# Kernel optimization log

Measured on AMD Instinct MI355X. Metric: run time of the kernel, lower is better.

## Reference

```python
import jax, jax.numpy as jnp
import numpy as np

N = 65536    # collocation points
N1 = 1024    # RBF centers
EPS = 0.1    # multiscale parameter used for width init scale


def setup_inputs() -> dict:
    key = jax.random.key(0)
    ks = jax.random.split(key, 10)
    x = jax.random.uniform(ks[0], (N, 2), dtype=jnp.float32)

    def mk(i):
        h = jax.random.uniform(ks[3 * i + 1], (N1,), dtype=jnp.float32)
        c = jax.random.uniform(ks[3 * i + 2], (N1, 2), dtype=jnp.float32)
        w = 5.0 * jax.random.uniform(ks[3 * i + 3], (N1, 2), dtype=jnp.float32) / EPS
        return h, c, w

    h1, c1, w1 = mk(0)
    h2, c2, w2 = mk(1)
    h3, c3, w3 = mk(2)
    return dict(x=x, hight=h1, center=c1, width=w1,
                hight2=h2, center2=c2, width2=w2,
                hight3=h3, center3=c3, width3=w3)


def _rbf(X, c, h, w):
    """Gaussian RBF expansion. X:(N,2) points, c:(N1,2) centers,
    h:(N1,) heights, w:(N1,2) widths. Returns u, du/dx, du/dy, each (N,)."""
    x1 = X[:, 0:1] - c[None, :, 0]          # (N, N1)
    y1 = X[:, 1:2] - c[None, :, 1]          # (N, N1)
    d1 = w[:, 0] ** 2                        # (N1,)
    d2 = w[:, 1] ** 2                        # (N1,)
    e = jnp.exp(-(x1 ** 2) * d1 - (y1 ** 2) * d2)  # (N, N1)
    u = e @ h                                # (N,)
    ux = (-2.0 * x1 * d1 * e) @ h            # (N,)
    uy = (-2.0 * y1 * d2 * e) @ h            # (N,)
    return u, ux, uy


def reference(x, hight, center, width, hight2, center2, width2,
              hight3, center3, width3):
    _, ux, uy = _rbf(x, center, hight, width)
    P, Px, _ = _rbf(x, center2, hight2, width2)
    Q, _, Qy = _rbf(x, center3, hight3, width3)
    return (ux, uy, P, Px, Q, Qy)
```

## Files before the change

### kernel.cpp

```cpp
#include <hip/hip_runtime.h>
#include <math.h>

#define N_PTS  65536
#define N_CTR  1024
#define CHUNK  128
#define PPT    4
#define PPB    (256 * PPT)

#if __has_builtin(__builtin_amdgcn_exp2f)
#define EXP2(v) __builtin_amdgcn_exp2f(v)
#else
#define EXP2(v) exp2f(v)
#endif


__global__ __launch_bounds__(256) void prep_kernel(
    const float* __restrict__ h0, const float* __restrict__ c0, const float* __restrict__ w0,
    const float* __restrict__ h1, const float* __restrict__ c1, const float* __restrict__ w1,
    const float* __restrict__ h2, const float* __restrict__ c2, const float* __restrict__ w2,
    float4* __restrict__ RA, float4* __restrict__ RB, float* __restrict__ RC,
    float4* __restrict__ out_zero)
{
    const int idx = blockIdx.x * 256 + threadIdx.x;

    {
        float4 z = make_float4(0.f, 0.f, 0.f, 0.f);
        float4* o = out_zero + idx * 32;
        #pragma unroll
        for (int t = 0; t < 32; ++t) o[t] = z;
    }

    if (idx >= 3 * N_CTR) return;
    const int set = idx >> 10;
    const int j   = idx & (N_CTR - 1);

    const float*  h = (set == 0) ? h0 : ((set == 1) ? h1 : h2);
    const float2* c = (const float2*)((set == 0) ? c0 : ((set == 1) ? c1 : c2));
    const float2* w = (const float2*)((set == 0) ? w0 : ((set == 1) ? w1 : w2));

    const float LOG2E = 1.4426950408889634f;
    float2 cj = c[j];
    float2 wj = w[j];
    float  hh = h[j];
    float d1 = wj.x * wj.x;
    float d2 = wj.y * wj.y;
    float zb =  2.f * cj.x * d1 * LOG2E;
    float zc = -d1 * LOG2E;
    float zd =  2.f * cj.y * d2 * LOG2E;
    float ze = -d2 * LOG2E;
    float za = -(cj.x * cj.x * d1 + cj.y * cj.y * d2) * LOG2E;
    float k0, k1, k2, k3;
    if (set == 0) {
        k0 = -2.f * hh * d1;  k1 = 2.f * hh * d1 * cj.x;
        k2 = -2.f * hh * d2;  k3 = 2.f * hh * d2 * cj.y;
    } else if (set == 1) {
        k0 = hh;  k1 = -2.f * hh * d1;  k2 = 2.f * hh * d1 * cj.x;  k3 = 0.f;
    } else {
        k0 = hh;  k1 = -2.f * hh * d2;  k2 = 2.f * hh * d2 * cj.y;  k3 = 0.f;
    }
    RA[idx] = make_float4(zb, zc, zd, ze);
    RB[idx] = make_float4(za, k0, k1, k2);
    RC[idx] = k3;
}

__global__ __launch_bounds__(256, 6) void srbf_main(
    const float* __restrict__ x,
    const float4* __restrict__ RA,
    const float4* __restrict__ RB,
    const float*  __restrict__ RC,
    float* __restrict__ out)
{
    const int bid   = blockIdx.x;
    const int set   = bid >> 9;
    const int r     = bid & 511;
    const int chunk = r >> 6;
    const int pblk  = r & 63;
    const int tid   = threadIdx.x;
    const int cbase = set * N_CTR + chunk * CHUNK;

    const int base = pblk * PPB + tid;
    float X[PPT], Y[PPT];
    #pragma unroll
    for (int p = 0; p < PPT; ++p) {
        float2 q = ((const float2*)x)[base + p * 256];
        X[p] = q.x;  Y[p] = q.y;
    }

    if (set == 0) {
        float A0[PPT], A1[PPT], A2[PPT], A3[PPT];
        #pragma unroll
        for (int p = 0; p < PPT; ++p) { A0[p] = A1[p] = A2[p] = A3[p] = 0.f; }

        #pragma unroll 4
        for (int jj = 0; jj < CHUNK; ++jj) {
            const float4 A  = RA[cbase + jj];
            const float4 B  = RB[cbase + jj];
            const float  k3 = RC[cbase + jj];
            float e[PPT];
            #pragma unroll
            for (int p = 0; p < PPT; ++p) {
                float t1 = fmaf(X[p], A.y, A.x);
                float t2 = fmaf(X[p], t1,  B.x);
                float t3 = fmaf(Y[p], A.w, A.z);
                float s  = fmaf(Y[p], t3,  t2);
                e[p] = EXP2(s);
            }
            #pragma unroll
            for (int p = 0; p < PPT; ++p) {
                A0[p] = fmaf(B.y, e[p], A0[p]);
                A1[p] = fmaf(B.z, e[p], A1[p]);
                A2[p] = fmaf(B.w, e[p], A2[p]);
                A3[p] = fmaf(k3,  e[p], A3[p]);
            }
        }
        #pragma unroll
        for (int p = 0; p < PPT; ++p) {
            const int i = base + p * 256;
            atomicAdd(&out[i],         fmaf(X[p], A0[p], A1[p]));
            atomicAdd(&out[N_PTS + i], fmaf(Y[p], A2[p], A3[p]));
        }
    } else {
        float A0[PPT], A1[PPT], A2[PPT];
        #pragma unroll
        for (int p = 0; p < PPT; ++p) { A0[p] = A1[p] = A2[p] = 0.f; }

        #pragma unroll 4
        for (int jj = 0; jj < CHUNK; ++jj) {
            const float4 A = RA[cbase + jj];
            const float4 B = RB[cbase + jj];
            float e[PPT];
            #pragma unroll
            for (int p = 0; p < PPT; ++p) {
                float t1 = fmaf(X[p], A.y, A.x);
                float t2 = fmaf(X[p], t1,  B.x);
                float t3 = fmaf(Y[p], A.w, A.z);
                float s  = fmaf(Y[p], t3,  t2);
                e[p] = EXP2(s);
            }
            #pragma unroll
            for (int p = 0; p < PPT; ++p) {
                A0[p] = fmaf(B.y, e[p], A0[p]);
                A1[p] = fmaf(B.z, e[p], A1[p]);
                A2[p] = fmaf(B.w, e[p], A2[p]);
            }
        }
        float* o = out + (size_t)set * 2 * N_PTS;
        #pragma unroll
        for (int p = 0; p < PPT; ++p) {
            const int i = base + p * 256;
            const float g = (set == 1) ? X[p] : Y[p];
            atomicAdd(&o[i],         A0[p]);
            atomicAdd(&o[N_PTS + i], fmaf(g, A1[p], A2[p]));
        }
    }
}

extern "C" void kernel_launch(void* const* d_in, const int* in_sizes, int n_in,
                              void* d_out, int out_size, void* d_ws, size_t ws_size,
                              hipStream_t stream) {
    const float* x  = (const float*)d_in[0];
    const float* h1 = (const float*)d_in[1];
    const float* c1 = (const float*)d_in[2];
    const float* w1 = (const float*)d_in[3];
    const float* h2 = (const float*)d_in[4];
    const float* c2 = (const float*)d_in[5];
    const float* w2 = (const float*)d_in[6];
    const float* h3 = (const float*)d_in[7];
    const float* c3 = (const float*)d_in[8];
    const float* w3 = (const float*)d_in[9];

    char* ws = (char*)d_ws;
    float4* RA = (float4*)(ws);
    float4* RB = (float4*)(ws + 49152);
    float*  RC = (float*) (ws + 98304);

    prep_kernel<<<dim3(12), dim3(256), 0, stream>>>(
        h1, c1, w1, h2, c2, w2, h3, c3, w3, RA, RB, RC, (float4*)d_out);

    srbf_main<<<dim3(1536), dim3(256), 0, stream>>>(x, RA, RB, RC, (float*)d_out);
}
```

Measured before the change: 60.73 us.

## Fuse center precompute into main kernel via shared memory, memset output

```diff
diff --git a/kernel.cpp b/kernel.cpp
--- a/kernel.cpp
+++ b/kernel.cpp
@@ -6,6 +6,7 @@
 #define CHUNK  128
 #define PPT    4
 #define PPB    (256 * PPT)
+#define LOG2E  1.4426950408889634f
 
 #if __has_builtin(__builtin_amdgcn_exp2f)
 #define EXP2(v) __builtin_amdgcn_exp2f(v)
@@ -13,70 +14,52 @@
 #define EXP2(v) exp2f(v)
 #endif
 
-
-__global__ __launch_bounds__(256) void prep_kernel(
+__global__ __launch_bounds__(256) void srbf_main(
+    const float* __restrict__ x,
     const float* __restrict__ h0, const float* __restrict__ c0, const float* __restrict__ w0,
     const float* __restrict__ h1, const float* __restrict__ c1, const float* __restrict__ w1,
     const float* __restrict__ h2, const float* __restrict__ c2, const float* __restrict__ w2,
-    float4* __restrict__ RA, float4* __restrict__ RB, float* __restrict__ RC,
-    float4* __restrict__ out_zero)
-{
-    const int idx = blockIdx.x * 256 + threadIdx.x;
-
-    {
-        float4 z = make_float4(0.f, 0.f, 0.f, 0.f);
-        float4* o = out_zero + idx * 32;
-        #pragma unroll
-        for (int t = 0; t < 32; ++t) o[t] = z;
-    }
-
-    if (idx >= 3 * N_CTR) return;
-    const int set = idx >> 10;
-    const int j   = idx & (N_CTR - 1);
-
-    const float*  h = (set == 0) ? h0 : ((set == 1) ? h1 : h2);
-    const float2* c = (const float2*)((set == 0) ? c0 : ((set == 1) ? c1 : c2));
-    const float2* w = (const float2*)((set == 0) ? w0 : ((set == 1) ? w1 : w2));
-
-    const float LOG2E = 1.4426950408889634f;
-    float2 cj = c[j];
-    float2 wj = w[j];
-    float  hh = h[j];
-    float d1 = wj.x * wj.x;
-    float d2 = wj.y * wj.y;
-    float zb =  2.f * cj.x * d1 * LOG2E;
-    float zc = -d1 * LOG2E;
-    float zd =  2.f * cj.y * d2 * LOG2E;
-    float ze = -d2 * LOG2E;
-    float za = -(cj.x * cj.x * d1 + cj.y * cj.y * d2) * LOG2E;
-    float k0, k1, k2, k3;
-    if (set == 0) {
-        k0 = -2.f * hh * d1;  k1 = 2.f * hh * d1 * cj.x;
-        k2 = -2.f * hh * d2;  k3 = 2.f * hh * d2 * cj.y;
-    } else if (set == 1) {
-        k0 = hh;  k1 = -2.f * hh * d1;  k2 = 2.f * hh * d1 * cj.x;  k3 = 0.f;
-    } else {
-        k0 = hh;  k1 = -2.f * hh * d2;  k2 = 2.f * hh * d2 * cj.y;  k3 = 0.f;
-    }
-    RA[idx] = make_float4(zb, zc, zd, ze);
-    RB[idx] = make_float4(za, k0, k1, k2);
-    RC[idx] = k3;
-}
-
-__global__ __launch_bounds__(256, 6) void srbf_main(
-    const float* __restrict__ x,
-    const float4* __restrict__ RA,
-    const float4* __restrict__ RB,
-    const float*  __restrict__ RC,
     float* __restrict__ out)
 {
+    __shared__ float4 sA[CHUNK];
+    __shared__ float4 sK[CHUNK];
+    __shared__ float  sk3[CHUNK];
+
     const int bid   = blockIdx.x;
     const int set   = bid >> 9;
     const int r     = bid & 511;
     const int chunk = r >> 6;
     const int pblk  = r & 63;
     const int tid   = threadIdx.x;
-    const int cbase = set * N_CTR + chunk * CHUNK;
+
+    if (tid < CHUNK) {
+        const int j = chunk * CHUNK + tid;
+        const float*  h = (set == 0) ? h0 : ((set == 1) ? h1 : h2);
+        const float2* c = (const float2*)((set == 0) ? c0 : ((set == 1) ? c1 : c2));
+        const float2* w = (const float2*)((set == 0) ? w0 : ((set == 1) ? w1 : w2));
+        float2 cj = c[j];
+        float2 wj = w[j];
+        float  hh = h[j];
+        float d1 = wj.x * wj.x;
+        float d2 = wj.y * wj.y;
+        float zb =  2.f * cj.x * d1 * LOG2E;
+        float zc = -d1 * LOG2E;
+        float zd =  2.f * cj.y * d2 * LOG2E;
+        float ze = -d2 * LOG2E;
+        float za = -(cj.x * cj.x * d1 + cj.y * cj.y * d2) * LOG2E;
+        float k0, k1, k2, k3;
+        if (set == 0) {
+            k0 = -2.f * hh * d1;  k1 = 2.f * hh * d1 * cj.x;
+            k2 = -2.f * hh * d2;  k3 = 2.f * hh * d2 * cj.y;
+        } else if (set == 1) {
+            k0 = hh;  k1 = -2.f * hh * d1;  k2 = 2.f * hh * d1 * cj.x;  k3 = 0.f;
+        } else {
+            k0 = hh;  k1 = -2.f * hh * d2;  k2 = 2.f * hh * d2 * cj.y;  k3 = 0.f;
+        }
+        sA[tid]  = make_float4(zb, zc, zd, ze);
+        sK[tid]  = make_float4(za, k0, k1, k2);
+        sk3[tid] = k3;
+    }
 
     const int base = pblk * PPB + tid;
     float X[PPT], Y[PPT];
@@ -85,6 +68,7 @@
         float2 q = ((const float2*)x)[base + p * 256];
         X[p] = q.x;  Y[p] = q.y;
     }
+    __syncthreads();
 
     if (set == 0) {
         float A0[PPT], A1[PPT], A2[PPT], A3[PPT];
@@ -92,24 +76,24 @@
         for (int p = 0; p < PPT; ++p) { A0[p] = A1[p] = A2[p] = A3[p] = 0.f; }
 
         #pragma unroll 4
-        for (int jj = 0; jj < CHUNK; ++jj) {
-            const float4 A  = RA[cbase + jj];
-            const float4 B  = RB[cbase + jj];
-            const float  k3 = RC[cbase + jj];
+        for (int j = 0; j < CHUNK; ++j) {
+            const float4 A  = sA[j];
+            const float4 K  = sK[j];
+            const float  k3 = sk3[j];
             float e[PPT];
             #pragma unroll
             for (int p = 0; p < PPT; ++p) {
                 float t1 = fmaf(X[p], A.y, A.x);
-                float t2 = fmaf(X[p], t1,  B.x);
+                float t2 = fmaf(X[p], t1,  K.x);
                 float t3 = fmaf(Y[p], A.w, A.z);
                 float s  = fmaf(Y[p], t3,  t2);
                 e[p] = EXP2(s);
             }
             #pragma unroll
             for (int p = 0; p < PPT; ++p) {
-                A0[p] = fmaf(B.y, e[p], A0[p]);
-                A1[p] = fmaf(B.z, e[p], A1[p]);
-                A2[p] = fmaf(B.w, e[p], A2[p]);
+                A0[p] = fmaf(K.y, e[p], A0[p]);
+                A1[p] = fmaf(K.z, e[p], A1[p]);
+                A2[p] = fmaf(K.w, e[p], A2[p]);
                 A3[p] = fmaf(k3,  e[p], A3[p]);
             }
         }
@@ -125,23 +109,23 @@
         for (int p = 0; p < PPT; ++p) { A0[p] = A1[p] = A2[p] = 0.f; }
 
         #pragma unroll 4
-        for (int jj = 0; jj < CHUNK; ++jj) {
-            const float4 A = RA[cbase + jj];
-            const float4 B = RB[cbase + jj];
+        for (int j = 0; j < CHUNK; ++j) {
+            const float4 A = sA[j];
+            const float4 K = sK[j];
             float e[PPT];
             #pragma unroll
             for (int p = 0; p < PPT; ++p) {
                 float t1 = fmaf(X[p], A.y, A.x);
-                float t2 = fmaf(X[p], t1,  B.x);
+                float t2 = fmaf(X[p], t1,  K.x);
                 float t3 = fmaf(Y[p], A.w, A.z);
                 float s  = fmaf(Y[p], t3,  t2);
                 e[p] = EXP2(s);
             }
             #pragma unroll
             for (int p = 0; p < PPT; ++p) {
-                A0[p] = fmaf(B.y, e[p], A0[p]);
-                A1[p] = fmaf(B.z, e[p], A1[p]);
-                A2[p] = fmaf(B.w, e[p], A2[p]);
+                A0[p] = fmaf(K.y, e[p], A0[p]);
+                A1[p] = fmaf(K.z, e[p], A1[p]);
+                A2[p] = fmaf(K.w, e[p], A2[p]);
             }
         }
         float* o = out + (size_t)set * 2 * N_PTS;
@@ -169,13 +153,8 @@
     const float* c3 = (const float*)d_in[8];
     const float* w3 = (const float*)d_in[9];
 
-    char* ws = (char*)d_ws;
-    float4* RA = (float4*)(ws);
-    float4* RB = (float4*)(ws + 49152);
-    float*  RC = (float*) (ws + 98304);
+    hipMemsetAsync(d_out, 0, (size_t)out_size * sizeof(float), stream);
 
-    prep_kernel<<<dim3(12), dim3(256), 0, stream>>>(
-        h1, c1, w1, h2, c2, w2, h3, c3, w3, RA, RB, RC, (float4*)d_out);
-
-    srbf_main<<<dim3(1536), dim3(256), 0, stream>>>(x, RA, RB, RC, (float*)d_out);
+    srbf_main<<<dim3(1536), dim3(256), 0, stream>>>(
+        x, h1, c1, w1, h2, c2, w2, h3, c3, w3, (float*)d_out);
 }
```

Measured after the change: 52.27 us. -13.9%, faster.
